# Kernel optimization log

Measured on AMD Instinct MI355X. Metric: run time of the kernel, lower is better.

Reference implementation:

```python
import jax, jax.numpy as jnp
import numpy as np

H_HEADS = 32
KV_HEADS = 8
HEAD_DIM = 64  # hidden // num_heads = 2048 // 32


def setup_inputs() -> dict:
    key = jax.random.key(0)
    ks = jax.random.split(key, 5)
    B, T, hidden = 2, 2048, 2048
    kv_dim = KV_HEADS * HEAD_DIM
    s = 0.02
    return {
        "x": jax.random.normal(ks[0], (B, T, hidden), dtype=jnp.float32),
        "Wq": jax.random.normal(ks[1], (hidden, hidden), dtype=jnp.float32) * s,
        "Wk": jax.random.normal(ks[2], (hidden, kv_dim), dtype=jnp.float32) * s,
        "Wv": jax.random.normal(ks[3], (hidden, kv_dim), dtype=jnp.float32) * s,
        "Wo": jax.random.normal(ks[4], (hidden, hidden), dtype=jnp.float32) * s,
    }


def reference(x, Wq, Wk, Wv, Wo):
    B, T, hidden = x.shape
    h, kv, d = H_HEADS, KV_HEADS, HEAD_DIM
    g = h // kv  # GQA group size
    scale = d ** (-0.5)

    # projections
    q = (x @ Wq).reshape(B, T, h, d).transpose(0, 2, 1, 3)        # [B,h,T,d]
    k = (x @ Wk).reshape(B, T, kv, d).transpose(0, 2, 1, 3)      # [B,kv,T,d]
    v = (x @ Wv).reshape(B, T, kv, d).transpose(0, 2, 1, 3)      # [B,kv,T,d]

    # native GQA broadcast: group q heads by their shared kv head
    # (equivalent math to torch repeat_interleave on k/v)
    qg = q.reshape(B, kv, g, T, d)                                # [B,kv,g,T,d]
    scores = jnp.einsum("bkgtd,bksd->bkgts", qg, k) * scale       # [B,kv,g,T,T]
    attn = jax.nn.softmax(scores, axis=-1)
    og = jnp.einsum("bkgts,bksd->bkgtd", attn, v)                 # [B,kv,g,T,d]
    out = og.reshape(B, h, T, d).transpose(0, 2, 1, 3).reshape(B, T, h * d)
    return out @ Wo
```

## Files before the change

kernel.cpp:

```cpp
#include <hip/hip_runtime.h>

#define AS1 __attribute__((address_space(1)))
#define AS3 __attribute__((address_space(3)))

typedef unsigned short u16;
typedef unsigned int u32;
typedef __attribute__((ext_vector_type(8))) _Float16 half8;
typedef __attribute__((ext_vector_type(2))) _Float16 half2v;
typedef __attribute__((ext_vector_type(4))) u16 u16x4;
typedef __attribute__((ext_vector_type(8))) u16 u16x8;
typedef __attribute__((ext_vector_type(4))) u32 u32x4;
typedef __attribute__((ext_vector_type(4))) float f32x4;
typedef __attribute__((ext_vector_type(16))) float f32x16;

__device__ __forceinline__ u16 f2h(float f) {
    _Float16 h = (_Float16)f;
    return __builtin_bit_cast(u16, h);
}

__device__ __forceinline__ u32 pk2h(float a, float b) {
    return __builtin_bit_cast(u32, __builtin_amdgcn_cvt_pkrtz(a, b));
}

__device__ __forceinline__ float fexp2(float x) {
#if __has_builtin(__builtin_amdgcn_exp2f)
    return __builtin_amdgcn_exp2f(x);
#else
    return __expf(x * 0.69314718055994531f);
#endif
}

__device__ __forceinline__ float dot2acc(u32 w, float acc) {
#if __has_builtin(__builtin_amdgcn_fdot2)
    half2v ones = { (_Float16)1.f, (_Float16)1.f };
    return __builtin_amdgcn_fdot2(__builtin_bit_cast(half2v, w), ones, acc, false);
#else
    half2v p = __builtin_bit_cast(half2v, w);
    return acc + (float)p[0] + (float)p[1];
#endif
}

__device__ __forceinline__ void plswap(u32& a, u32& b) {
    asm("v_permlane32_swap_b32 %0, %1" : "+v"(a), "+v"(b));
}

__device__ __forceinline__ void async16(const void* g, void* l) {
    __builtin_amdgcn_global_load_lds((AS1 void*)g, (AS3 void*)l, 16, 0, 0);
}


__global__ void prep_inputs(const float* __restrict__ x, u16* __restrict__ xb,
                            const float* __restrict__ Wq, const float* __restrict__ Wk,
                            const float* __restrict__ Wv, const float* __restrict__ Wo,
                            u16* __restrict__ Wqt, u16* __restrict__ Wkvt,
                            u16* __restrict__ Wot, float qscale) {
    __shared__ float tile[32][33];
    const int z = blockIdx.z;
    if (z == 4) {
        size_t base = ((size_t)(blockIdx.y * 64 + blockIdx.x) * 256 + threadIdx.x) * 8;
        float4 v0 = *(const float4*)(x + base);
        float4 v1 = *(const float4*)(x + base + 4);
        u16x8 o = { f2h(v0.x), f2h(v0.y), f2h(v0.z), f2h(v0.w),
                    f2h(v1.x), f2h(v1.y), f2h(v1.z), f2h(v1.w) };
        *(u16x8*)(xb + base) = o;
        return;
    }
    const float* in;
    u16* out;
    int N;
    float scale = 1.f;
    if (z == 0)      { in = Wq; out = Wqt; N = 2048; scale = qscale; }
    else if (z == 1) { in = Wo; out = Wot; N = 2048; }
    else if (z == 2) { in = Wk; out = Wkvt; N = 512; }
    else             { in = Wv; out = Wkvt + (size_t)512 * 2048; N = 512; }
    const int K = 2048;
    int nb = blockIdx.x * 32, kb = blockIdx.y * 32;
    if (nb >= N) return;
    int tx = threadIdx.x & 31, ty = threadIdx.x >> 5;
#pragma unroll
    for (int r = ty; r < 32; r += 8)
        tile[r][tx] = in[(size_t)(kb + r) * N + nb + tx];
    __syncthreads();
#pragma unroll
    for (int r = ty; r < 32; r += 8)
        out[(size_t)(nb + r) * K + kb + tx] = f2h(tile[tx][r] * scale);
}


template <int OUTMODE>
__global__ __launch_bounds__(256, OUTMODE == 3 ? 3 : 2) void gemm_bt(
        const u16* __restrict__ A, const u16* __restrict__ Bt,
        void* __restrict__ C, void* __restrict__ C2,
        int M, int N, int K, int ldc) {
    __shared__ __align__(16) u16 As[3][128 * 32];
    __shared__ __align__(16) u16 Bs[3][128 * 32];
    const int bid = blockIdx.y * gridDim.x + blockIdx.x;
    const int cpx = (gridDim.x * gridDim.y) >> 3;
    const int swzid = (bid & 7) * cpx + (bid >> 3);
    const int bx = swzid % gridDim.x, by = swzid / gridDim.x;

    const int m0 = bx * 128, n0 = by * 128;
    const int wave = threadIdx.x >> 6, lane = threadIdx.x & 63;
    const int quad = lane >> 4, mm = lane & 15;
    const int wm = (wave >> 1) * 64, wn = (wave & 1) * 64;

    const int srow = wave * 16 + (lane >> 2);
    const int scol = 8 * ((lane & 3) ^ ((lane >> 3) & 3));

    const u16* ag0 = A + (size_t)(m0 + srow) * K + scol;
    const u16* ag1 = A + (size_t)(m0 + 64 + srow) * K + scol;
    const u16* bg0 = Bt + (size_t)(n0 + srow) * K + scol;
    const u16* bg1 = Bt + (size_t)(n0 + 64 + srow) * K + scol;
    const int soff = wave * 512 + lane * 8;

    f32x4 acc[4][4] = {};
    const int swz = (mm >> 1) & 3;

#define GST(buf)                                                              \
    {                                                                         \
        u16* ad = &As[buf][soff];                                             \
        u16* bd = &Bs[buf][soff];                                             \
        async16(ag0, ad);                                                     \
        async16(ag1, ad + 2048);                                              \
        async16(bg0, bd);                                                     \
        async16(bg1, bd + 2048);                                              \
        ag0 += 32; ag1 += 32; bg0 += 32; bg1 += 32;                           \
    }

    GST(0);
    GST(1);
    int cur = 0;

    for (int k0 = 0; k0 < K; k0 += 32) {
        if (k0 + 32 < K) {
            asm volatile("s_waitcnt vmcnt(4)" ::: "memory");
        } else {
            asm volatile("s_waitcnt vmcnt(0)" ::: "memory");
        }
        __builtin_amdgcn_s_barrier();
        if (k0 + 64 < K) {
            int nb = cur + 2;
            if (nb >= 3) nb -= 3;
            GST(nb);
        }
        const u16* Ac = &As[cur][0];
        const u16* Bc = &Bs[cur][0];
        half8 af[4], bf[4];
#pragma unroll
        for (int i = 0; i < 4; i++)
            af[i] = *(const half8*)(Ac + (wm + i * 16 + mm) * 32 + (quad ^ swz) * 8);
#pragma unroll
        for (int i = 0; i < 4; i++)
            bf[i] = *(const half8*)(Bc + (wn + i * 16 + mm) * 32 + (quad ^ swz) * 8);
#pragma unroll
        for (int mi = 0; mi < 4; mi++)
#pragma unroll
            for (int ni = 0; ni < 4; ni++)
                acc[mi][ni] = __builtin_amdgcn_mfma_f32_16x16x32_f16(
                    af[mi], bf[ni], acc[mi][ni], 0, 0, 0);
        if (++cur == 3) cur = 0;
    }
#undef GST

    if (OUTMODE == 0) {
        float* Cp = (float*)C;
#pragma unroll
        for (int mi = 0; mi < 4; mi++)
#pragma unroll
            for (int r = 0; r < 4; r++) {
                float* rp = Cp + (size_t)(m0 + wm + mi * 16 + quad * 4 + r) * ldc + n0 + wn + mm;
#pragma unroll
                for (int ni = 0; ni < 4; ni++) rp[ni * 16] = acc[mi][ni][r];
            }
    } else if (OUTMODE == 1) {
        u16* Cp = (u16*)C;
#pragma unroll
        for (int mi = 0; mi < 4; mi++)
#pragma unroll
            for (int r = 0; r < 4; r++) {
                u16* rp = Cp + (size_t)(m0 + wm + mi * 16 + quad * 4 + r) * ldc + n0 + wn + mm;
#pragma unroll
                for (int ni = 0; ni < 4; ni++) rp[ni * 16] = f2h(acc[mi][ni][r]);
            }
    } else if (OUTMODE == 2) {
        u16* Cp = (u16*)C;
#pragma unroll
        for (int mi = 0; mi < 4; mi++)
#pragma unroll
            for (int ni = 0; ni < 4; ni++) {
                int col = n0 + wn + ni * 16 + mm;
                int row0 = m0 + wm + mi * 16 + quad * 4;
                u16x4 o = { f2h(acc[mi][ni][0]), f2h(acc[mi][ni][1]),
                            f2h(acc[mi][ni][2]), f2h(acc[mi][ni][3]) };
                *(u16x4*)((u16*)Cp + (size_t)col * ldc + row0) = o;
            }
    } else {
        if (n0 < 2048) {
            u16* Qp = (u16*)C;
#pragma unroll
            for (int mi = 0; mi < 4; mi++)
#pragma unroll
                for (int r = 0; r < 4; r++) {
                    u16* rp = Qp + (size_t)(m0 + wm + mi * 16 + quad * 4 + r) * 2048 + n0 + wn + mm;
#pragma unroll
                    for (int ni = 0; ni < 4; ni++) rp[ni * 16] = f2h(acc[mi][ni][r]);
                }
        } else if (n0 < 2560) {
            u16* Kp = (u16*)C2;
#pragma unroll
            for (int mi = 0; mi < 4; mi++)
#pragma unroll
                for (int r = 0; r < 4; r++) {
                    u16* rp = Kp + (size_t)(m0 + wm + mi * 16 + quad * 4 + r) * 512 + (n0 - 2048) + wn + mm;
#pragma unroll
                    for (int ni = 0; ni < 4; ni++) rp[ni * 16] = f2h(acc[mi][ni][r]);
                }
        } else {
            u16* Vp = (u16*)C2 + (size_t)4096 * 512;
#pragma unroll
            for (int mi = 0; mi < 4; mi++)
#pragma unroll
                for (int ni = 0; ni < 4; ni++) {
                    int col = n0 - 2560 + wn + ni * 16 + mm;
                    int row0 = m0 + wm + mi * 16 + quad * 4;
                    u16x4 o = { f2h(acc[mi][ni][0]), f2h(acc[mi][ni][1]),
                                f2h(acc[mi][ni][2]), f2h(acc[mi][ni][3]) };
                    *(u16x4*)(Vp + (size_t)col * 4096 + row0) = o;
                }
        }
    }
}


template <int SPLIT>
__global__ __launch_bounds__(512, 4) void attn_fwd(const u16* __restrict__ Qb,
                                                   const u16* __restrict__ Kb,
                                                   const u16* __restrict__ Vtb,
                                                   u16* __restrict__ Ob,
                                                   float* __restrict__ Of0,
                                                   float* __restrict__ Of1,
                                                   float* __restrict__ Lf) {
    __shared__ __align__(16) u16 Ks[2][64 * 64];
    __shared__ __align__(16) u16 Vs[2][64 * 64];

    const int qtb = blockIdx.x, head = blockIdx.y;
    const int b = blockIdx.z & 1, sp = blockIdx.z >> 1;
    const int kvh = head >> 2;
    const int wave = threadIdx.x >> 6, lane = threadIdx.x & 63;
    const int h = lane >> 5;
    const int q32 = lane & 31;
    const int t = threadIdx.x;

    const size_t qrow0 = (size_t)b * 2048 + qtb * 256 + wave * 32;
    const int s_beg = sp * (2048 / SPLIT), s_end = s_beg + 2048 / SPLIT;

    half8 qf[4];
#pragma unroll
    for (int s = 0; s < 4; s++)
        qf[s] = *(const half8*)(Qb + (qrow0 + q32) * 2048 + head * 64 + s * 16 + h * 8);

    f32x16 accO[2] = {};
    float lpq[4] = {0.f, 0.f, 0.f, 0.f};

    f32x16 NEG10;
#pragma unroll
    for (int i = 0; i < 16; i++) NEG10[i] = -10.f;

    const int srow = t >> 3;
    const int lch = (t & 7) ^ (srow & 7);
    const u16* kg = Kb + ((size_t)b * 2048 + srow) * 512 + kvh * 64 + lch * 8;
    const u16* vg = Vtb + ((size_t)kvh * 64 + srow) * 4096 + b * 2048 + lch * 8;

#define STAGE(buf, s0)                                                        \
    {                                                                         \
        async16(kg + (size_t)(s0) * 512, &Ks[buf][t * 8]);                    \
        async16(vg + (s0), &Vs[buf][t * 8]);                                  \
    }

    int cur = 0;
    STAGE(0, s_beg);

    const int r0 = q32, r1 = 32 + q32;
    const int sw0 = (r0 & 7), sw1 = (r1 & 7);

    for (int s0 = s_beg; s0 < s_end; s0 += 64) {
        __syncthreads();
        int sn = s0 + 64;
        if (sn < s_end) STAGE(cur ^ 1, sn);

        const u16* Kc = &Ks[cur][0];
        const u16* Vc = &Vs[cur][0];
        const u16* Kr0 = Kc + r0 * 64;
        const u16* Kr1 = Kc + r1 * 64;

        f32x16 a0, a1;
        __builtin_amdgcn_s_setprio(1);
        {
            half8 k0 = *(const half8*)(Kr0 + ((h ^ sw0) << 3));
            a0 = __builtin_amdgcn_mfma_f32_32x32x16_f16(k0, qf[0], NEG10, 0, 0, 0);
            half8 k1 = *(const half8*)(Kr1 + ((h ^ sw1) << 3));
            a1 = __builtin_amdgcn_mfma_f32_32x32x16_f16(k1, qf[0], NEG10, 0, 0, 0);
        }
#pragma unroll
        for (int s = 1; s < 4; s++) {
            half8 k0 = *(const half8*)(Kr0 + (((2 * s + h) ^ sw0) << 3));
            a0 = __builtin_amdgcn_mfma_f32_32x32x16_f16(k0, qf[s], a0, 0, 0, 0);
            half8 k1 = *(const half8*)(Kr1 + (((2 * s + h) ^ sw1) << 3));
            a1 = __builtin_amdgcn_mfma_f32_32x32x16_f16(k1, qf[s], a1, 0, 0, 0);
        }
        __builtin_amdgcn_s_setprio(0);

        u32 w0[8];
#pragma unroll
        for (int m = 0; m < 8; m++) {
            w0[m] = pk2h(fexp2(a0[2 * m]), fexp2(a0[2 * m + 1]));
            lpq[m & 3] = dot2acc(w0[m], lpq[m & 3]);
        }

        __builtin_amdgcn_s_setprio(1);
#pragma unroll
        for (int k1 = 0; k1 < 2; k1++) {
            const int ks = k1;
            u32 d0 = w0[4 * k1 + 0], d2 = w0[4 * k1 + 2];
            u32 d1 = w0[4 * k1 + 1], d3 = w0[4 * k1 + 3];
            plswap(d0, d2);
            plswap(d1, d3);
            u32x4 pd = { d0, d1, d2, d3 };
            half8 pf = __builtin_bit_cast(half8, pd);
#pragma unroll
            for (int dt = 0; dt < 2; dt++) {
                const int rv = dt * 32 + q32;
                half8 vf = *(const half8*)(&Vc[rv * 64 + (((2 * ks + h) ^ (rv & 7)) << 3)]);
                accO[dt] = __builtin_amdgcn_mfma_f32_32x32x16_f16(vf, pf, accO[dt], 0, 0, 0);
            }
        }
        __builtin_amdgcn_s_setprio(0);

        u32 w1[8];
#pragma unroll
        for (int m = 0; m < 8; m++) {
            w1[m] = pk2h(fexp2(a1[2 * m]), fexp2(a1[2 * m + 1]));
            lpq[m & 3] = dot2acc(w1[m], lpq[m & 3]);
        }

        __builtin_amdgcn_s_setprio(1);
#pragma unroll
        for (int k1 = 0; k1 < 2; k1++) {
            const int ks = 2 + k1;
            u32 d0 = w1[4 * k1 + 0], d2 = w1[4 * k1 + 2];
            u32 d1 = w1[4 * k1 + 1], d3 = w1[4 * k1 + 3];
            plswap(d0, d2);
            plswap(d1, d3);
            u32x4 pd = { d0, d1, d2, d3 };
            half8 pf = __builtin_bit_cast(half8, pd);
#pragma unroll
            for (int dt = 0; dt < 2; dt++) {
                const int rv = dt * 32 + q32;
                half8 vf = *(const half8*)(&Vc[rv * 64 + (((2 * ks + h) ^ (rv & 7)) << 3)]);
                accO[dt] = __builtin_amdgcn_mfma_f32_32x32x16_f16(vf, pf, accO[dt], 0, 0, 0);
            }
        }
        __builtin_amdgcn_s_setprio(0);

        cur ^= 1;
    }
#undef STAGE

    float l = (lpq[0] + lpq[1]) + (lpq[2] + lpq[3]);
    l += __shfl_xor(l, 32);

    const size_t token = qrow0 + q32;
    if (SPLIT == 1) {
        float inv = 1.f / l;
#pragma unroll
        for (int dt = 0; dt < 2; dt++)
#pragma unroll
            for (int rq = 0; rq < 4; rq++) {
                u16x4 o = { f2h(accO[dt][4 * rq + 0] * inv), f2h(accO[dt][4 * rq + 1] * inv),
                            f2h(accO[dt][4 * rq + 2] * inv), f2h(accO[dt][4 * rq + 3] * inv) };
                *(u16x4*)(Ob + token * 2048 + head * 64 + dt * 32 + rq * 8 + h * 4) = o;
            }
    } else {
        float* Op = sp ? Of1 : Of0;
#pragma unroll
        for (int dt = 0; dt < 2; dt++)
#pragma unroll
            for (int rq = 0; rq < 4; rq++) {
                f32x4 o = { accO[dt][4 * rq + 0], accO[dt][4 * rq + 1],
                            accO[dt][4 * rq + 2], accO[dt][4 * rq + 3] };
                *(f32x4*)(Op + token * 2048 + head * 64 + dt * 32 + rq * 8 + h * 4) = o;
            }
        if (!h) Lf[((size_t)sp * 4096 + token) * 32 + head] = l;
    }
}


extern "C" void kernel_launch(void* const* d_in, const int* in_sizes, int n_in,
                              void* d_out, int out_size, void* d_ws, size_t ws_size,
                              hipStream_t stream) {
    (void)in_sizes; (void)n_in; (void)out_size; (void)ws_size;
    const float* x  = (const float*)d_in[0];
    const float* Wq = (const float*)d_in[1];
    const float* Wk = (const float*)d_in[2];
    const float* Wv = (const float*)d_in[3];
    const float* Wo = (const float*)d_in[4];
    float* out = (float*)d_out;

    u16* ws = (u16*)d_ws;
    u16* xb   = ws;
    u16* Wqt  = xb   + (size_t)4096 * 2048;
    u16* Wkvt = Wqt  + (size_t)2048 * 2048;
    u16* Wot  = Wkvt + (size_t)1024 * 2048;
    u16* Qb   = Wot  + (size_t)2048 * 2048;
    u16* Kb   = Qb   + (size_t)4096 * 2048;
    u16* Vtb  = Kb   + (size_t)4096 * 512;
    u16* Ob   = Vtb  + (size_t)512 * 4096;

    const float qscale = 0.125f * 1.4426950408889634f;

    prep_inputs<<<dim3(64, 64, 5), 256, 0, stream>>>(x, xb, Wq, Wk, Wv, Wo,
                                                     Wqt, Wkvt, Wot, qscale);

    gemm_bt<3><<<dim3(32, 24), 256, 0, stream>>>(xb, Wqt, Qb, Kb, 4096, 3072, 2048, 2048);

    attn_fwd<1><<<dim3(8, 32, 2), 512, 0, stream>>>(Qb, Kb, Vtb, Ob,
                                                    nullptr, nullptr, nullptr);

    gemm_bt<0><<<dim3(32, 16), 256, 0, stream>>>(Ob, Wot, out, nullptr, 4096, 2048, 2048, 2048);
}
```

Baseline: 315.3 us.

## Add dedicated output-projection GEMM with 64-wide K tiles and vectorize weight transpose loads

Replaces the generic gemm_bt<0> used for the Wo projection with a specialized kernel that stages 128x64 K-tiles, double-buffered and XOR-swizzled in LDS. It uses the 16x16x32 f16 MFMA and writes fp32 output directly. This halves the number of K iterations and barriers per tile, at the cost of more LDS per block. Separately, the weight transpose prep now reads each row with one float4 load per thread instead of four scalar strided loads.

```diff
diff --git a/kernel.cpp b/kernel.cpp
--- a/kernel.cpp
+++ b/kernel.cpp
@@ -76,11 +76,14 @@
     const int K = 2048;
     int nb = blockIdx.x * 32, kb = blockIdx.y * 32;
     if (nb >= N) return;
+    {
+        int r = threadIdx.x >> 3, c4 = (threadIdx.x & 7) * 4;
+        float4 v = *(const float4*)(in + (size_t)(kb + r) * N + nb + c4);
+        tile[r][c4 + 0] = v.x; tile[r][c4 + 1] = v.y;
+        tile[r][c4 + 2] = v.z; tile[r][c4 + 3] = v.w;
+    }
+    __syncthreads();
     int tx = threadIdx.x & 31, ty = threadIdx.x >> 5;
-#pragma unroll
-    for (int r = ty; r < 32; r += 8)
-        tile[r][tx] = in[(size_t)(kb + r) * N + nb + tx];
-    __syncthreads();
 #pragma unroll
     for (int r = ty; r < 32; r += 8)
         out[(size_t)(nb + r) * K + kb + tx] = f2h(tile[tx][r] * scale);
@@ -232,6 +235,82 @@
 }
 
 
+__global__ __launch_bounds__(256, 2) void gemm_wo(
+        const u16* __restrict__ A, const u16* __restrict__ Bt,
+        float* __restrict__ C, int M, int N, int K, int ldc) {
+    __shared__ __align__(16) u16 As[2][128 * 64];
+    __shared__ __align__(16) u16 Bs[2][128 * 64];
+    const int bid = blockIdx.y * gridDim.x + blockIdx.x;
+    const int cpx = (gridDim.x * gridDim.y) >> 3;
+    const int swzid = (bid & 7) * cpx + (bid >> 3);
+    const int bx = swzid % gridDim.x, by = swzid / gridDim.x;
+
+    const int m0 = bx * 128, n0 = by * 128;
+    const int wave = threadIdx.x >> 6, lane = threadIdx.x & 63;
+    const int quad = lane >> 4, mm = lane & 15;
+    const int wm = (wave >> 1) * 64, wn = (wave & 1) * 64;
+    const int t = threadIdx.x;
+
+    const int srow = t >> 3;
+    const int lch = (t & 7) ^ (srow & 7);
+    const u16* ag = A + (size_t)(m0 + srow) * K + lch * 8;
+    const u16* bg = Bt + (size_t)(n0 + srow) * K + lch * 8;
+    const int d8 = t * 8;
+
+    f32x4 acc[4][4] = {};
+    const int swb = mm & 7;
+
+#define GSTW(buf)                                                             \
+    {                                                                         \
+        _Pragma("unroll")                                                     \
+        for (int p = 0; p < 4; p++) {                                         \
+            async16(ag + (size_t)(p * 32) * K, &As[buf][d8 + p * 2048]);      \
+            async16(bg + (size_t)(p * 32) * K, &Bs[buf][d8 + p * 2048]);      \
+        }                                                                     \
+        ag += 64; bg += 64;                                                   \
+    }
+
+    GSTW(0);
+    int cur = 0;
+
+    for (int k0 = 0; k0 < K; k0 += 64) {
+        __syncthreads();
+        if (k0 + 64 < K) GSTW(cur ^ 1);
+        const u16* Ac = &As[cur][0];
+        const u16* Bc = &Bs[cur][0];
+#pragma unroll
+        for (int kk = 0; kk < 2; kk++) {
+            half8 af[4], bf[4];
+#pragma unroll
+            for (int i = 0; i < 4; i++)
+                af[i] = *(const half8*)(Ac + (wm + i * 16 + mm) * 64 +
+                                        (((kk * 4 + quad) ^ swb) << 3));
+#pragma unroll
+            for (int i = 0; i < 4; i++)
+                bf[i] = *(const half8*)(Bc + (wn + i * 16 + mm) * 64 +
+                                        (((kk * 4 + quad) ^ swb) << 3));
+#pragma unroll
+            for (int mi = 0; mi < 4; mi++)
+#pragma unroll
+                for (int ni = 0; ni < 4; ni++)
+                    acc[mi][ni] = __builtin_amdgcn_mfma_f32_16x16x32_f16(
+                        af[mi], bf[ni], acc[mi][ni], 0, 0, 0);
+        }
+        cur ^= 1;
+    }
+#undef GSTW
+
+#pragma unroll
+    for (int mi = 0; mi < 4; mi++)
+#pragma unroll
+        for (int r = 0; r < 4; r++) {
+            float* rp = C + (size_t)(m0 + wm + mi * 16 + quad * 4 + r) * ldc + n0 + wn + mm;
+#pragma unroll
+            for (int ni = 0; ni < 4; ni++) rp[ni * 16] = acc[mi][ni][r];
+        }
+}
+
+
 template <int SPLIT>
 __global__ __launch_bounds__(512, 4) void attn_fwd(const u16* __restrict__ Qb,
                                                    const u16* __restrict__ Kb,
@@ -426,5 +505,5 @@
     attn_fwd<1><<<dim3(8, 32, 2), 512, 0, stream>>>(Qb, Kb, Vtb, Ob,
                                                     nullptr, nullptr, nullptr);
 
-    gemm_bt<0><<<dim3(32, 16), 256, 0, stream>>>(Ob, Wot, out, nullptr, 4096, 2048, 2048, 2048);
-}
+    gemm_wo<<<dim3(32, 16), 256, 0, stream>>>(Ob, Wot, out, 4096, 2048, 2048, 2048);
+}
```

Measured after the change: 296.6 us. 1.06x faster.
